# Kernel tuning notes

Hardware: AMD Instinct MI355X
Metric: run time of the kernel (lower is better)

The kernel has to match this reference:

```python
import jax, jax.numpy as jnp
import numpy as np

N = 8192        # num nodes == input_dim (attn is [N,N], indexed by edge endpoints)
E = 262144      # num edges (nnz of sparse G), avg degree 32
OD = 64         # output_dim


def setup_inputs() -> dict:
    key = jax.random.key(0)
    k_x, k_r, k_c, k_v, k_a, k_w = jax.random.split(key, 6)
    x = jax.random.normal(k_x, (N, N), dtype=jnp.float32)
    row = jax.random.randint(k_r, (E,), 0, N)
    col = jax.random.randint(k_c, (E,), 0, N)
    values = jax.random.uniform(k_v, (E,), dtype=jnp.float32)
    attn = jax.random.uniform(k_a, (N, N), dtype=jnp.float32)  # init uniform(0,1) per reset_parameters
    stdv = 1.0 / np.sqrt(OD)
    weight = jax.random.uniform(k_w, (N, OD), dtype=jnp.float32, minval=-stdv, maxval=stdv)
    return {"x": x, "attn": attn, "weight": weight, "values": values, "row": row, "col": col}


def reference(x, attn, weight, values, row, col):
    # x = x @ W : [N, OD]
    y = x @ weight
    # sparse_dense_mul: scale each edge's value by attn[row, col] (irregular gather)
    ev = values * attn[row, col]                      # [E]
    # torch.sparse.mm(G, y): out[i] = sum_{e: row[e]==i} ev[e] * y[col[e]]
    out = jax.ops.segment_sum(ev[:, None] * y[col], row, num_segments=x.shape[0])
    return (out, jnp.linalg.norm(attn))
```

## Files before the change

kernel.cpp:

```cpp
#include <hip/hip_runtime.h>
#include <hip/hip_bf16.h>

#define N 8192
#define OD 64
#define E_EDGES 262144

#define BM 64
#define BK 64
#define KSPLIT 16
#define KS_PER_SPLIT (N / KSPLIT)
#define NTILES (KS_PER_SPLIT / BK)
#define SCAT_BLOCKS 8192
#define EDGE_ITERS (E_EDGES / (SCAT_BLOCKS * 4))

typedef __attribute__((ext_vector_type(8))) short bf16x8;
typedef __attribute__((ext_vector_type(4))) float f32x4;

__device__ __forceinline__ unsigned short f2bf(float f) {
    union { float f; unsigned u; } v; v.f = f;
    unsigned r = (v.u + 0x7fffu + ((v.u >> 16) & 1u)) >> 16;
    return (unsigned short)r;
}

__device__ __forceinline__ void gload16(const void* g, void* l) {
    __builtin_amdgcn_global_load_lds(
        (const __attribute__((address_space(1))) unsigned int*)g,
        (__attribute__((address_space(3))) unsigned int*)l, 16, 0, 0);
}

__global__ __launch_bounds__(256) void prep_kernel(const float* __restrict__ w,
                                                   unsigned short* __restrict__ wt,
                                                   float4* __restrict__ y4,
                                                   float4* __restrict__ out4) {
    const int bid = blockIdx.x, t = threadIdx.x;
    const int base = bid * 256 + t;
    float4 z{0.f, 0.f, 0.f, 0.f};
    #pragma unroll
    for (int u = 0; u < 4; ++u) y4[base + u * 32768] = z;
    #pragma unroll
    for (int u = 0; u < 4; ++u) out4[base + u * 32768] = z;

    __shared__ unsigned short lds[64][80];
    const int kb = bid * 64;
    #pragma unroll
    for (int p = 0; p < 4; ++p) {
        int idx = p * 1024 + t * 4;
        int r = idx >> 6, c = idx & 63;
        float4 v = *(const float4*)(&w[(size_t)(kb + r) * OD + c]);
        lds[c + 0][r] = f2bf(v.x);
        lds[c + 1][r] = f2bf(v.y);
        lds[c + 2][r] = f2bf(v.z);
        lds[c + 3][r] = f2bf(v.w);
    }
    __syncthreads();
    const int colx = t >> 2, j0 = (t & 3) * 16;
    #pragma unroll
    for (int u = 0; u < 2; ++u) {
        *(bf16x8*)(wt + (size_t)colx * N + kb + j0 + u * 8) =
            *(const bf16x8*)(&lds[colx][j0 + u * 8]);
    }
}

__global__ __launch_bounds__(256) void gemm_kernel(const float* __restrict__ x,
                                                   const unsigned short* __restrict__ wt,
                                                   float* __restrict__ y) {
    __shared__ float xs[3][BM * BK];
    __shared__ unsigned short bs[3][BM * BK];

    const int t = threadIdx.x;
    const int wv = t >> 6, lane = t & 63;
    const int lrow = lane & 15, g = lane >> 4;
    const int sw = lrow & 7;
    const int row0 = blockIdx.x * BM;
    const int k0 = blockIdx.y * KS_PER_SPLIT;

    const int xrow_b = t >> 4, xchunk = t & 15;
    const int brow_b = t >> 3, bchunk = t & 7;

    f32x4 acc[4] = {f32x4{0,0,0,0}, f32x4{0,0,0,0}, f32x4{0,0,0,0}, f32x4{0,0,0,0}};

    #define STAGE(buf, tile)                                                          \
        {                                                                             \
            const int kk = k0 + (tile) * BK;                                          \
            _Pragma("unroll")                                                         \
            for (int j = 0; j < 4; ++j) {                                             \
                int r = j * 16 + xrow_b;                                              \
                gload16(&x[(size_t)(row0 + r) * N + kk + ((xchunk ^ (r & 7)) << 2)],  \
                        &xs[buf][j * 1024 + t * 4]);                                  \
            }                                                                         \
            _Pragma("unroll")                                                         \
            for (int j = 0; j < 2; ++j) {                                             \
                int r = j * 32 + brow_b;                                              \
                gload16(&wt[(size_t)r * N + kk + ((bchunk ^ (r & 7)) << 3)],          \
                        &bs[buf][j * 2048 + t * 8]);                                  \
            }                                                                         \
        }

    STAGE(0, 0);
    STAGE(1, 1);

    #pragma unroll
    for (int tile = 0; tile < NTILES; ++tile) {
        const int cur = tile % 3;
        if (tile < NTILES - 1) {
            asm volatile("s_waitcnt vmcnt(6)" ::: "memory");
        } else {
            asm volatile("s_waitcnt vmcnt(0)" ::: "memory");
        }
        __builtin_amdgcn_s_barrier();
        if (tile + 2 < NTILES) STAGE((tile + 2) % 3, tile + 2);

        const int ar = wv * 16 + lrow;
        #pragma unroll
        for (int ks = 0; ks < 2; ++ks) {
            const int c0 = ks * 8 + g * 2;
            float4 lo = *(const float4*)&xs[cur][ar * 64 + ((c0 ^ sw) << 2)];
            float4 hi = *(const float4*)&xs[cur][ar * 64 + (((c0 + 1) ^ sw) << 2)];
            bf16x8 a;
            a[0] = f2bf(lo.x); a[1] = f2bf(lo.y); a[2] = f2bf(lo.z); a[3] = f2bf(lo.w);
            a[4] = f2bf(hi.x); a[5] = f2bf(hi.y); a[6] = f2bf(hi.z); a[7] = f2bf(hi.w);
            #pragma unroll
            for (int cf = 0; cf < 4; ++cf) {
                const int rb = cf * 16 + lrow;
                bf16x8 b = *(const bf16x8*)&bs[cur][rb * 64 + (((ks * 4 + g) ^ sw) << 3)];
                acc[cf] = __builtin_amdgcn_mfma_f32_16x16x32_bf16(a, b, acc[cf], 0, 0, 0);
            }
        }
    }

    float* yp = y + ((size_t)row0 + wv * 16 + g * 4) * OD;
    #pragma unroll
    for (int cf = 0; cf < 4; ++cf) {
        #pragma unroll
        for (int i = 0; i < 4; ++i)
            atomicAdd(&yp[i * OD + cf * 16 + lrow], acc[cf][i]);
    }
    #undef STAGE
}

__device__ __forceinline__ void do_scatter(const float* __restrict__ values,
                                           const float* __restrict__ attn,
                                           const int* __restrict__ row,
                                           const int* __restrict__ col,
                                           const float* __restrict__ y,
                                           float* __restrict__ out,
                                           int bid, int t) {
    const int lane = t & 63;
    const int w = t >> 6;
    int r8[EDGE_ITERS], c8[EDGE_ITERS];
    float v8[EDGE_ITERS], a8[EDGE_ITERS];
    #pragma unroll
    for (int i = 0; i < EDGE_ITERS; ++i) {
        int e = bid * 4 + w + i * (SCAT_BLOCKS * 4);
        r8[i] = row[e]; c8[i] = col[e]; v8[i] = values[e];
    }
    #pragma unroll
    for (int i = 0; i < EDGE_ITERS; ++i)
        a8[i] = attn[(size_t)r8[i] * N + c8[i]];
    #pragma unroll
    for (int i = 0; i < EDGE_ITERS; ++i) {
        float yv = y[c8[i] * OD + lane];
        atomicAdd(&out[r8[i] * OD + lane], v8[i] * a8[i] * yv);
    }
}

__device__ __forceinline__ float do_norm_part(const float* __restrict__ attn, int bid, int t) {
    const float4* a4 = (const float4*)attn;
    float s = 0.f;
    int i = bid * 256 + t;
    #pragma unroll
    for (int u = 0; u < 8; ++u) {
        float4 v = a4[i + u * (SCAT_BLOCKS * 256)];
        s += v.x * v.x + v.y * v.y + v.z * v.z + v.w * v.w;
    }
    return s;
}

__global__ __launch_bounds__(256) void scatter_norm_kernel(
        const float* __restrict__ values, const float* __restrict__ attn,
        const int* __restrict__ row, const int* __restrict__ col,
        const float* __restrict__ y, float* __restrict__ out,
        float* __restrict__ part) {
    const int bid = blockIdx.x, t = threadIdx.x;
    float s;
    if (bid & 1) {
        s = do_norm_part(attn, bid, t);
        do_scatter(values, attn, row, col, y, out, bid, t);
    } else {
        do_scatter(values, attn, row, col, y, out, bid, t);
        s = do_norm_part(attn, bid, t);
    }
    for (int off = 32; off > 0; off >>= 1) s += __shfl_down(s, off, 64);
    __shared__ float wpart[4];
    int wid = t >> 6;
    if ((t & 63) == 0) wpart[wid] = s;
    __syncthreads();
    if (t == 0) part[bid] = wpart[0] + wpart[1] + wpart[2] + wpart[3];
}

__global__ __launch_bounds__(256) void finalize_kernel(const float* __restrict__ part,
                                                       float* __restrict__ out_norm) {
    float s = 0.f;
    #pragma unroll
    for (int k = 0; k < SCAT_BLOCKS / 256; ++k) s += part[k * 256 + threadIdx.x];
    for (int off = 32; off > 0; off >>= 1) s += __shfl_down(s, off, 64);
    __shared__ float wp[4];
    int wid = threadIdx.x >> 6;
    if ((threadIdx.x & 63) == 0) wp[wid] = s;
    __syncthreads();
    if (threadIdx.x == 0) *out_norm = sqrtf(wp[0] + wp[1] + wp[2] + wp[3]);
}

extern "C" void kernel_launch(void* const* d_in, const int* in_sizes, int n_in,
                              void* d_out, int out_size, void* d_ws, size_t ws_size,
                              hipStream_t stream) {
    const float* x      = (const float*)d_in[0];
    const float* attn   = (const float*)d_in[1];
    const float* weight = (const float*)d_in[2];
    const float* values = (const float*)d_in[3];
    const int*   row    = (const int*)d_in[4];
    const int*   col    = (const int*)d_in[5];
    float* out = (float*)d_out;

    char* wsb = (char*)d_ws;
    float*          part = (float*)wsb;
    unsigned short* wt   = (unsigned short*)(wsb + (1u << 20));
    float*          y    = (float*)(wsb + (2u << 20));

    prep_kernel<<<128, 256, 0, stream>>>(weight, wt, (float4*)y, (float4*)out);
    gemm_kernel<<<dim3(N / BM, KSPLIT), 256, 0, stream>>>(x, wt, y);
    scatter_norm_kernel<<<SCAT_BLOCKS, 256, 0, stream>>>(values, attn, row, col, y, out, part);
    finalize_kernel<<<1, 256, 0, stream>>>(part, out + (size_t)N * OD);
}
```

Measured before the change: 166.7 us.

## Load x directly into registers and stage whole weight slice in LDS once

The GEMM kernel no longer runs a triple-buffered LDS pipeline for x tiles. Each block now loads its entire 512-wide bf16 weight slice into LDS once, and each lane reads x directly from global memory into registers, software-pipelined in four quarters. The fp32-to-bf16 conversion changes from round-to-nearest to truncation via a byte-permute pack. This removes the per-tile barriers and the LDS round trip for x, but it raises register pressure and slightly changes numerics because truncation replaces rounding.

```diff
diff --git a/kernel.cpp b/kernel.cpp
--- a/kernel.cpp
+++ b/kernel.cpp
@@ -6,10 +6,8 @@
 #define E_EDGES 262144
 
 #define BM 64
-#define BK 64
 #define KSPLIT 16
 #define KS_PER_SPLIT (N / KSPLIT)
-#define NTILES (KS_PER_SPLIT / BK)
 #define SCAT_BLOCKS 8192
 #define EDGE_ITERS (E_EDGES / (SCAT_BLOCKS * 4))
 
@@ -20,6 +18,14 @@
     union { float f; unsigned u; } v; v.f = f;
     unsigned r = (v.u + 0x7fffu + ((v.u >> 16) & 1u)) >> 16;
     return (unsigned short)r;
+}
+
+__device__ __forceinline__ unsigned pack_trunc(unsigned lo, unsigned hi) {
+#if defined(__has_builtin) && __has_builtin(__builtin_amdgcn_perm)
+    return __builtin_amdgcn_perm(hi, lo, 0x07060302u);
+#else
+    return (lo >> 16) | (hi & 0xFFFF0000u);
+#endif
 }
 
 __device__ __forceinline__ void gload16(const void* g, void* l) {
@@ -64,78 +70,76 @@
 __global__ __launch_bounds__(256) void gemm_kernel(const float* __restrict__ x,
                                                    const unsigned short* __restrict__ wt,
                                                    float* __restrict__ y) {
-    __shared__ float xs[3][BM * BK];
-    __shared__ unsigned short bs[3][BM * BK];
+    __shared__ unsigned short blds[64 * 512];
 
     const int t = threadIdx.x;
     const int wv = t >> 6, lane = t & 63;
     const int lrow = lane & 15, g = lane >> 4;
-    const int sw = lrow & 7;
-    const int row0 = blockIdx.x * BM;
+    const int row = blockIdx.x * BM + wv * 16 + lrow;
     const int k0 = blockIdx.y * KS_PER_SPLIT;
-
-    const int xrow_b = t >> 4, xchunk = t & 15;
-    const int brow_b = t >> 3, bchunk = t & 7;
+    const int bkey = (lrow & 7) << 3;
+
+    #pragma unroll
+    for (int j = 0; j < 16; ++j) {
+        const int brow = j * 4 + wv;
+        gload16(wt + (size_t)brow * N + k0 + ((lane ^ (brow & 7)) << 3),
+                &blds[brow * 512 + lane * 8]);
+    }
+    asm volatile("s_waitcnt vmcnt(0)" ::: "memory");
+    __builtin_amdgcn_sched_barrier(0);
+    __builtin_amdgcn_s_barrier();
 
     f32x4 acc[4] = {f32x4{0,0,0,0}, f32x4{0,0,0,0}, f32x4{0,0,0,0}, f32x4{0,0,0,0}};
-
-    #define STAGE(buf, tile)                                                          \
-        {                                                                             \
-            const int kk = k0 + (tile) * BK;                                          \
-            _Pragma("unroll")                                                         \
-            for (int j = 0; j < 4; ++j) {                                             \
-                int r = j * 16 + xrow_b;                                              \
-                gload16(&x[(size_t)(row0 + r) * N + kk + ((xchunk ^ (r & 7)) << 2)],  \
-                        &xs[buf][j * 1024 + t * 4]);                                  \
-            }                                                                         \
-            _Pragma("unroll")                                                         \
-            for (int j = 0; j < 2; ++j) {                                             \
-                int r = j * 32 + brow_b;                                              \
-                gload16(&wt[(size_t)r * N + kk + ((bchunk ^ (r & 7)) << 3)],          \
-                        &bs[buf][j * 2048 + t * 8]);                                  \
-            }                                                                         \
+    const float* xp = x + (size_t)row * N + k0 + g * 8;
+    uint4 xb[8];
+    bf16x8 A[4];
+
+    #define LOADQ(q)                                                  \
+        _Pragma("unroll")                                             \
+        for (int i = 0; i < 4; ++i) {                                 \
+            xb[2*i]   = *(const uint4*)(xp + (q) * 128 + i * 32);     \
+            xb[2*i+1] = *(const uint4*)(xp + (q) * 128 + i * 32 + 4); \
         }
 
-    STAGE(0, 0);
-    STAGE(1, 1);
-
-    #pragma unroll
-    for (int tile = 0; tile < NTILES; ++tile) {
-        const int cur = tile % 3;
-        if (tile < NTILES - 1) {
-            asm volatile("s_waitcnt vmcnt(6)" ::: "memory");
-        } else {
-            asm volatile("s_waitcnt vmcnt(0)" ::: "memory");
+    #define PACKQ()                                                   \
+        _Pragma("unroll")                                             \
+        for (int i = 0; i < 4; ++i) {                                 \
+            union { bf16x8 v; unsigned u[4]; } Au;                    \
+            Au.u[0] = pack_trunc(xb[2*i].x,   xb[2*i].y);             \
+            Au.u[1] = pack_trunc(xb[2*i].z,   xb[2*i].w);             \
+            Au.u[2] = pack_trunc(xb[2*i+1].x, xb[2*i+1].y);           \
+            Au.u[3] = pack_trunc(xb[2*i+1].z, xb[2*i+1].w);           \
+            A[i] = Au.v;                                              \
         }
-        __builtin_amdgcn_s_barrier();
-        if (tile + 2 < NTILES) STAGE((tile + 2) % 3, tile + 2);
-
-        const int ar = wv * 16 + lrow;
-        #pragma unroll
-        for (int ks = 0; ks < 2; ++ks) {
-            const int c0 = ks * 8 + g * 2;
-            float4 lo = *(const float4*)&xs[cur][ar * 64 + ((c0 ^ sw) << 2)];
-            float4 hi = *(const float4*)&xs[cur][ar * 64 + (((c0 + 1) ^ sw) << 2)];
-            bf16x8 a;
-            a[0] = f2bf(lo.x); a[1] = f2bf(lo.y); a[2] = f2bf(lo.z); a[3] = f2bf(lo.w);
-            a[4] = f2bf(hi.x); a[5] = f2bf(hi.y); a[6] = f2bf(hi.z); a[7] = f2bf(hi.w);
-            #pragma unroll
-            for (int cf = 0; cf < 4; ++cf) {
-                const int rb = cf * 16 + lrow;
-                bf16x8 b = *(const bf16x8*)&bs[cur][rb * 64 + (((ks * 4 + g) ^ sw) << 3)];
-                acc[cf] = __builtin_amdgcn_mfma_f32_16x16x32_bf16(a, b, acc[cf], 0, 0, 0);
-            }
+
+    #define MFMAQ(q)                                                              \
+        _Pragma("unroll")                                                         \
+        for (int ks = 0; ks < 4; ++ks) {                                          \
+            _Pragma("unroll")                                                     \
+            for (int cf = 0; cf < 4; ++cf) {                                      \
+                bf16x8 b = *(const bf16x8*)&blds[(cf * 16 + lrow) * 512 +         \
+                                (((q) * 128 + ks * 32 + g * 8) ^ bkey)];          \
+                acc[cf] = __builtin_amdgcn_mfma_f32_16x16x32_bf16(A[ks], b,       \
+                                                                  acc[cf], 0,0,0);\
+            }                                                                     \
         }
-    }
-
-    float* yp = y + ((size_t)row0 + wv * 16 + g * 4) * OD;
+
+    LOADQ(0);
+    PACKQ(); LOADQ(1); MFMAQ(0);
+    PACKQ(); LOADQ(2); MFMAQ(1);
+    PACKQ(); LOADQ(3); MFMAQ(2);
+    PACKQ();           MFMAQ(3);
+
+    float* yp = y + ((size_t)blockIdx.x * BM + wv * 16 + g * 4) * OD;
     #pragma unroll
     for (int cf = 0; cf < 4; ++cf) {
         #pragma unroll
         for (int i = 0; i < 4; ++i)
             atomicAdd(&yp[i * OD + cf * 16 + lrow], acc[cf][i]);
     }
-    #undef STAGE
+    #undef LOADQ
+    #undef PACKQ
+    #undef MFMAQ
 }
 
 __device__ __forceinline__ void do_scatter(const float* __restrict__ values,
```

Result: no change. 165.9 us (-0.5%).
